# Kernel tuning notes

Hardware: AMD Instinct MI355X
Metric: run time of the kernel (lower is better)

## Reference

```python
import jax, jax.numpy as jnp
import numpy as np

B, N_LEAVES, HID, NCLS, VOCAB = 32, 512, 128, 2, 50257
N_NODES = 2 * N_LEAVES - 1  # complete binary tree, heap layout


def setup_inputs() -> dict:
    key = jax.random.key(0)
    ks = jax.random.split(key, 12)
    x = jax.random.randint(ks[0], (B, N_NODES), 0, VOCAB)
    cue = jax.random.randint(ks[1], (B, N_NODES), 0, NCLS)
    # word j sits at tree leaf node L-1+j
    word_index = jnp.tile(jnp.arange(N_LEAVES - 1, 2 * N_LEAVES - 1), (B, 1))
    # parent->child adjacency stored in adj[:, 1]
    A = np.zeros((2, N_NODES, N_NODES), dtype=bool)
    p = np.arange(N_LEAVES - 1)
    A[1, p, 2 * p + 1] = True
    A[1, p, 2 * p + 2] = True
    adj = jnp.asarray(np.broadcast_to(A, (B, 2, N_NODES, N_NODES)).copy())
    s = 0.05
    emb = jax.random.normal(ks[2], (VOCAB, HID - NCLS)) * s
    Wc = jax.random.normal(ks[3], (HID, 2 * HID)) * s
    bc = jax.random.normal(ks[4], (HID,)) * s
    Wd = jax.random.normal(ks[5], (2 * HID, 2 * HID)) * s
    bd = jax.random.normal(ks[6], (2 * HID,)) * s
    Wg = jax.random.normal(ks[7], (HID, HID)) * s
    bg = jax.random.normal(ks[8], (HID,)) * s
    Wcl = jax.random.normal(ks[9], (NCLS, 2 * HID)) * s
    bcl = jax.random.normal(ks[10], (NCLS,)) * s
    return dict(x=x, word_index=word_index, cue=cue, adj=adj, emb=emb,
                Wc=Wc, bc=bc, Wd=Wd, bd=bd, Wg=Wg, bg=bg, Wcl=Wcl, bcl=bcl)


def reference(x, word_index, cue, adj, emb, Wc, bc, Wd, bd, Wg, bg, Wcl, bcl):
    # adj encodes the same complete binary heap tree that is hardcoded below
    Bn, N = x.shape
    H = Wc.shape[0]
    C = bcl.shape[0]
    L = (N + 1) // 2
    depth = L.bit_length() - 1  # leaves live at level `depth`
    bidx = jnp.arange(Bn)[:, None]

    word_emb = emb[x]                                   # (B, N, H-C)
    cue_oh = jax.nn.one_hot(cue, C, dtype=word_emb.dtype)
    in_feats = jnp.concatenate([word_emb, cue_oh], -1)  # (B, N, H)
    sent = in_feats[bidx, word_index]                   # (B, L, H) leaf feats

    # ---- upward compose: level-batched bottom-up traversal ----
    h = jnp.zeros((Bn, N, H), in_feats.dtype).at[bidx, word_index].set(sent)
    for d in range(depth - 1, -1, -1):
        p = jnp.arange(2 ** d - 1, 2 ** (d + 1) - 1)
        ctx = jnp.concatenate([h[:, 2 * p + 1], h[:, 2 * p + 2]], -1)  # (B, 2^d, 2H)
        h = h.at[:, p].set(jnp.tanh(ctx @ Wc.T + bc))
    # upward_results never writes leaf rows -> leaves stay zero
    up = h.at[bidx, word_index].set(0.0)

    g_down = jax.nn.sigmoid(h[:, 0] @ Wg.T + bg)        # (B, H)

    # ---- downward decompose: level-batched top-down traversal ----
    down = jnp.zeros_like(h).at[:, 0].set(g_down)
    for d in range(depth):
        p = jnp.arange(2 ** d - 1, 2 ** (d + 1) - 1)
        ctx = jnp.concatenate([down[:, p], up[:, p]], -1)
        ch = jnp.tanh(ctx @ Wd.T + bd)                  # (B, 2^d, 2H)
        down = down.at[:, 2 * p + 1].set(ch[..., :H]).at[:, 2 * p + 2].set(ch[..., H:])

    tree = jnp.concatenate([down, up], -1)              # (B, N, 2H)
    scores = jax.nn.sigmoid(tree @ Wcl.T + bcl)
    return jax.nn.softmax(scores, -1)
```

## Files before the change

### kernel.cpp

```cpp
#include <hip/hip_runtime.h>


constexpr int NNODES = 1023;
constexpr int HB = 128;

__device__ __forceinline__ float fold16(const float* a, int l) {
  float b[8];
#pragma unroll
  for (int u = 0; u < 8; ++u) {
    const float mine = (l & 1) ? a[2 * u + 1] : a[2 * u];
    const float oth  = (l & 1) ? a[2 * u]     : a[2 * u + 1];
    b[u] = mine + __shfl_xor(oth, 1);
  }
  float c[4];
#pragma unroll
  for (int u = 0; u < 4; ++u) {
    const float mine = (l & 2) ? b[2 * u + 1] : b[2 * u];
    const float oth  = (l & 2) ? b[2 * u]     : b[2 * u + 1];
    c[u] = mine + __shfl_xor(oth, 2);
  }
  float d[2];
#pragma unroll
  for (int u = 0; u < 2; ++u) {
    const float mine = (l & 4) ? c[2 * u + 1] : c[2 * u];
    const float oth  = (l & 4) ? c[2 * u]     : c[2 * u + 1];
    d[u] = mine + __shfl_xor(oth, 4);
  }
  const float mine = (l & 8) ? d[1] : d[0];
  const float oth  = (l & 8) ? d[0] : d[1];
  return mine + __shfl_xor(oth, 8);
}

__device__ __forceinline__ float fold8(const float* a, int l) {
  float b[4];
#pragma unroll
  for (int u = 0; u < 4; ++u) {
    const float mine = (l & 1) ? a[2 * u + 1] : a[2 * u];
    const float oth  = (l & 1) ? a[2 * u]     : a[2 * u + 1];
    b[u] = mine + __shfl_xor(oth, 1);
  }
  float c[2];
#pragma unroll
  for (int u = 0; u < 2; ++u) {
    const float mine = (l & 2) ? b[2 * u + 1] : b[2 * u];
    const float oth  = (l & 2) ? b[2 * u]     : b[2 * u + 1];
    c[u] = mine + __shfl_xor(oth, 2);
  }
  const float mine = (l & 4) ? c[1] : c[0];
  const float oth  = (l & 4) ? c[0] : c[1];
  return mine + __shfl_xor(oth, 4);
}

__device__ __forceinline__ float fold4(const float* a, int l) {
  float b[2];
#pragma unroll
  for (int u = 0; u < 2; ++u) {
    const float mine = (l & 1) ? a[2 * u + 1] : a[2 * u];
    const float oth  = (l & 1) ? a[2 * u]     : a[2 * u + 1];
    b[u] = mine + __shfl_xor(oth, 1);
  }
  const float mine = (l & 2) ? b[1] : b[0];
  const float oth  = (l & 2) ? b[0] : b[1];
  return mine + __shfl_xor(oth, 2);
}

template<int CH>
__device__ __forceinline__ float foldCH(const float (&a)[CH * 4], int l16) {
  if constexpr (CH == 4) {
    return fold16(a, l16);
  } else if constexpr (CH == 2) {
    float t = fold8(a, l16);
    t += __shfl_xor(t, 8);
    return t;
  } else {
    float t = fold4(a, l16);
    t += __shfl_xor(t, 4);
    t += __shfl_xor(t, 8);
    return t;
  }
}

template<int CH>
__device__ __forceinline__ void up_pass(float* __restrict__ heap, int base, int cb,
                                        int cbase, const float4 (&w)[4][4],
                                        float bias_r, int g, int l16, bool wr) {
  float a[CH * 4];
#pragma unroll
  for (int v = 0; v < CH * 4; ++v) a[v] = 0.f;
#pragma unroll
  for (int p = 0; p < CH; ++p) {
    const float* cp = heap + (cb + 2 * (cbase + p)) * HB + l16 * 4;
#pragma unroll
    for (int m = 0; m < 4; ++m) {
      const float4 cc = *(const float4*)(cp + m * 64);
#pragma unroll
      for (int r = 0; r < 4; ++r) {
        const float4 wv = w[r][m];
        a[p * 4 + r] = fmaf(wv.x, cc.x, fmaf(wv.y, cc.y,
                        fmaf(wv.z, cc.z, fmaf(wv.w, cc.w, a[p * 4 + r]))));
      }
    }
  }
  const float tot = foldCH<CH>(a, l16);
  if (wr && l16 < CH * 4) {
    const int p = l16 >> 2;
    heap[(base + cbase + p) * HB + 4 * g + (l16 & 3)] = tanhf(tot + bias_r);
  }
}

template<int NP, int NH>
__device__ __forceinline__ void up_level16(float* __restrict__ heap,
                                           const float4 (&w)[4][4],
                                           float bias_r, int g, int l16, int ph) {
  constexpr int base = NP - 1, cb = 2 * NP - 1;
  if constexpr (NP >= 4 * NH) {
#pragma unroll
    for (int c0 = 0; c0 < NP; c0 += 4 * NH)
      up_pass<4>(heap, base, cb, c0 + ph * 4, w, bias_r, g, l16, true);
  } else if constexpr (NP * 2 == 4 * NH) {
    up_pass<2>(heap, base, cb, ph * 2, w, bias_r, g, l16, true);
  } else if constexpr (NP == NH) {
    up_pass<1>(heap, base, cb, ph, w, bias_r, g, l16, true);
  } else {
    up_pass<1>(heap, base, cb, 0, w, bias_r, g, l16, ph == 0);
  }
  __syncthreads();
}

template<int CH>
__device__ __forceinline__ void down_pass(float* __restrict__ db,
                                          const float* __restrict__ ub,
                                          int base, int cb, int cbase,
                                          const float4 (&w)[4][4],
                                          float bias_r, int g, int l16) {
  float a[CH * 4];
#pragma unroll
  for (int v = 0; v < CH * 4; ++v) a[v] = 0.f;
#pragma unroll
  for (int p = 0; p < CH; ++p) {
    const float* dp = db + (base + cbase + p) * HB + l16 * 4;
    const float* up = ub + (base + cbase + p) * HB + l16 * 4;
#pragma unroll
    for (int m = 0; m < 4; ++m) {
      const float4 cc = *(const float4*)(((m < 2) ? dp : up) + (m & 1) * 64);
#pragma unroll
      for (int r = 0; r < 4; ++r) {
        const float4 wv = w[r][m];
        a[p * 4 + r] = fmaf(wv.x, cc.x, fmaf(wv.y, cc.y,
                        fmaf(wv.z, cc.z, fmaf(wv.w, cc.w, a[p * 4 + r]))));
      }
    }
  }
  const float tot = foldCH<CH>(a, l16);
  if (l16 < CH * 4) {
    const int p = l16 >> 2;
    const int row = 4 * g + (l16 & 3);
    db[(cb + 2 * (cbase + p) + (row >> 7)) * HB + (row & 127)] = tanhf(tot + bias_r);
  }
}

template<int NP>
__device__ __forceinline__ void down_level16(float* __restrict__ db,
                                             const float* __restrict__ ub,
                                             const float4 (&w)[4][4],
                                             float bias_r, int g, int l16) {
  constexpr int base = NP - 1, cb = 2 * NP - 1;
  if constexpr (NP >= 4) {
#pragma unroll
    for (int c0 = 0; c0 < NP; c0 += 4)
      down_pass<4>(db, ub, base, cb, c0, w, bias_r, g, l16);
  } else {
    down_pass<NP>(db, ub, base, cb, 0, w, bias_r, g, l16);
  }
  __syncthreads();
}

__device__ __forceinline__ void classify16(const float* __restrict__ dn,
                                           const float* __restrict__ un,
                                           const float* __restrict__ wcl,
                                           const float* __restrict__ bcl,
                                           float* __restrict__ o, int l16) {
  const int k0 = l16 * 8;
  float s0, s1;
  {
    const float4 d0 = *(const float4*)(dn + k0);
    const float4 d1 = *(const float4*)(dn + k0 + 4);
    const float4 a0 = *(const float4*)(wcl + k0);
    const float4 a1 = *(const float4*)(wcl + k0 + 4);
    const float4 b0 = *(const float4*)(wcl + 256 + k0);
    const float4 b1 = *(const float4*)(wcl + 256 + k0 + 4);
    s0 = d0.x * a0.x + d0.y * a0.y + d0.z * a0.z + d0.w * a0.w
       + d1.x * a1.x + d1.y * a1.y + d1.z * a1.z + d1.w * a1.w;
    s1 = d0.x * b0.x + d0.y * b0.y + d0.z * b0.z + d0.w * b0.w
       + d1.x * b1.x + d1.y * b1.y + d1.z * b1.z + d1.w * b1.w;
  }
  if (un) {
    const float4 u0 = *(const float4*)(un + k0);
    const float4 u1 = *(const float4*)(un + k0 + 4);
    const float4 a0 = *(const float4*)(wcl + 128 + k0);
    const float4 a1 = *(const float4*)(wcl + 128 + k0 + 4);
    const float4 b0 = *(const float4*)(wcl + 384 + k0);
    const float4 b1 = *(const float4*)(wcl + 384 + k0 + 4);
    s0 += u0.x * a0.x + u0.y * a0.y + u0.z * a0.z + u0.w * a0.w
        + u1.x * a1.x + u1.y * a1.y + u1.z * a1.z + u1.w * a1.w;
    s1 += u0.x * b0.x + u0.y * b0.y + u0.z * b0.z + u0.w * b0.w
        + u1.x * b1.x + u1.y * b1.y + u1.z * b1.z + u1.w * b1.w;
  }
#pragma unroll
  for (int m = 8; m >= 1; m >>= 1) {
    s0 += __shfl_xor(s0, m);
    s1 += __shfl_xor(s1, m);
  }
  if (l16 == 0) {
    s0 += bcl[0]; s1 += bcl[1];
    const float p0 = 1.f / (1.f + expf(-s0));
    const float p1 = 1.f / (1.f + expf(-s1));
    const float mx = fmaxf(p0, p1);
    const float e0 = expf(p0 - mx), e1 = expf(p1 - mx);
    const float inv = 1.f / (e0 + e1);
    o[0] = e0 * inv;
    o[1] = e1 * inv;
  }
}

__global__ __launch_bounds__(512, 4) void kA_up(const int* __restrict__ x,
                                                const int* __restrict__ cue,
                                                const float* __restrict__ emb,
                                                const float* __restrict__ Wc,
                                                const float* __restrict__ bc,
                                                float* __restrict__ hw) {
  __shared__ __align__(16) float heap[63 * HB];
  __shared__ __align__(16) float pad[7296];
  const int b = blockIdx.x >> 4, s = blockIdx.x & 15, r = 15 + s;
  const int t = threadIdx.x, g = t >> 4, l16 = t & 15;
  if (t == 0) ((volatile float*)pad)[0] = 0.f;

  float4 w[4][4];
#pragma unroll
  for (int rr = 0; rr < 4; ++rr)
#pragma unroll
    for (int m = 0; m < 4; ++m)
      w[rr][m] = *(const float4*)(Wc + (4 * g + rr) * 256 + l16 * 4 + m * 64);
  const float bias_r = bc[4 * g + (l16 & 3)];

  for (int idx = t; idx < 32 * HB; idx += 512) {
    const int j = idx >> 7, k = idx & 127;
    const int gq = ((r + 1) << 5) - 1 + j;
    float v;
    if (k < 126) v = emb[(long long)x[b * NNODES + gq] * 126 + k];
    else         v = (cue[b * NNODES + gq] == (k - 126)) ? 1.f : 0.f;
    heap[(31 + j) * HB + k] = v;
  }
  __syncthreads();

  up_level16<16, 1>(heap, w, bias_r, g, l16, 0);
  up_level16<8, 1>(heap, w, bias_r, g, l16, 0);
  up_level16<4, 1>(heap, w, bias_r, g, l16, 0);
  up_level16<2, 1>(heap, w, bias_r, g, l16, 0);
  up_level16<1, 1>(heap, w, bias_r, g, l16, 0);

  float4* dst = (float4*)(hw + (size_t)(b * 16 + s) * 31 * HB);
  const float4* src = (const float4*)heap;
  for (int idx = t; idx < 31 * 32; idx += 512) dst[idx] = src[idx];
}

__global__ __launch_bounds__(1024, 4) void kC_all(const float* __restrict__ Wc,
                                                  const float* __restrict__ bc,
                                                  const float* __restrict__ Wg,
                                                  const float* __restrict__ bg,
                                                  const float* __restrict__ Wd,
                                                  const float* __restrict__ bd,
                                                  const float* __restrict__ Wcl,
                                                  const float* __restrict__ bcl,
                                                  const float* __restrict__ hw,
                                                  float* __restrict__ out) {
  __shared__ __align__(16) float A[63 * HB];
  __shared__ __align__(16) float B[31 * HB];
  __shared__ __align__(16) float rootdn[2 * HB];
  __shared__ __align__(16) float wcl[512];
  __shared__ __align__(16) float pad[7400];
  const int b = blockIdx.x >> 3, sp = blockIdx.x & 7;
  const int t = threadIdx.x, g = t >> 4, l16 = t & 15;
  if (t == 0) ((volatile float*)pad)[0] = 0.f;

  {
    float4* B4 = (float4*)(B + 15 * HB);
    for (int idx = t; idx < 16 * 32; idx += 1024) {
      const int s = idx >> 5, k4 = idx & 31;
      B4[idx] = ((const float4*)(hw + (size_t)(b * 16 + s) * 31 * HB))[k4];
    }
  }
  if (t < 512) wcl[t] = Wcl[t];
  __syncthreads();

  {
    const int gu = g & 31, ph = t >> 9;
    float4 w[4][4];
#pragma unroll
    for (int rr = 0; rr < 4; ++rr)
#pragma unroll
      for (int m = 0; m < 4; ++m)
        w[rr][m] = *(const float4*)(Wc + (4 * gu + rr) * 256 + l16 * 4 + m * 64);
    const float bias_r = bc[4 * gu + (l16 & 3)];
    up_level16<8, 2>(B, w, bias_r, gu, l16, ph);
    up_level16<4, 2>(B, w, bias_r, gu, l16, ph);
    up_level16<2, 2>(B, w, bias_r, gu, l16, ph);
    up_level16<1, 2>(B, w, bias_r, gu, l16, ph);

    float4 wg[4][2];
#pragma unroll
    for (int rr = 0; rr < 4; ++rr)
#pragma unroll
      for (int m = 0; m < 2; ++m)
        wg[rr][m] = *(const float4*)(Wg + (4 * gu + rr) * 128 + l16 * 4 + m * 64);
    float a[4];
#pragma unroll
    for (int v = 0; v < 4; ++v) a[v] = 0.f;
#pragma unroll
    for (int m = 0; m < 2; ++m) {
      const float4 cc = *(const float4*)(B + l16 * 4 + m * 64);
#pragma unroll
      for (int rr = 0; rr < 4; ++rr) {
        const float4 wv = wg[rr][m];
        a[rr] = fmaf(wv.x, cc.x, fmaf(wv.y, cc.y, fmaf(wv.z, cc.z, fmaf(wv.w, cc.w, a[rr]))));
      }
    }
    float tot = fold4(a, l16);
    tot += __shfl_xor(tot, 4);
    tot += __shfl_xor(tot, 8);
    if (ph == 0 && l16 < 4) {
      const int row = 4 * gu + l16;
      A[row] = 1.f / (1.f + expf(-(tot + bg[row])));
    }
    __syncthreads();
  }
  asm volatile("" ::: "memory");

  float4 w[4][4];
#pragma unroll
  for (int rr = 0; rr < 4; ++rr)
#pragma unroll
    for (int m = 0; m < 4; ++m)
      w[rr][m] = *(const float4*)(Wd + (4 * g + rr) * 256 + l16 * 4 + m * 64);
  const float bias_r = bd[4 * g + (l16 & 3)];

  down_level16<1>(A, B, w, bias_r, g, l16);
  down_level16<2>(A, B, w, bias_r, g, l16);
  down_level16<4>(A, B, w, bias_r, g, l16);
  down_level16<8>(A, B, w, bias_r, g, l16);

  if (sp == 0 && t < 15 * 16) {
    const int m = t >> 4;
    classify16(A + m * HB, B + m * HB, wcl, bcl,
               out + ((size_t)b * NNODES + m) * 2, l16);
  }
  if (t < 256) rootdn[t] = A[(15 + sp * 2 + (t >> 7)) * HB + (t & 127)];
  __syncthreads();

  for (int ss = 0; ss < 2; ++ss) {
    const int s = sp * 2 + ss, r = 15 + s;

    {
      const float4* s4 = (const float4*)(hw + (size_t)(b * 16 + s) * 31 * HB);
      float4* B4 = (float4*)B;
      for (int idx = t; idx < 31 * 32; idx += 1024) B4[idx] = s4[idx];
      if (t < HB) A[t] = rootdn[ss * HB + t];
    }
    __syncthreads();

    down_level16<1>(A, B, w, bias_r, g, l16);
    down_level16<2>(A, B, w, bias_r, g, l16);
    down_level16<4>(A, B, w, bias_r, g, l16);
    down_level16<8>(A, B, w, bias_r, g, l16);
    down_level16<16>(A, B, w, bias_r, g, l16);

    if (t < 63 * 16) {
      const int m = t >> 4;
      const int lvl = 31 - __clz(m + 1);
      const int j = (m + 1) - (1 << lvl);
      const int gq = ((r + 1) << lvl) - 1 + j;
      classify16(A + m * HB, (m < 31) ? (B + m * HB) : nullptr, wcl, bcl,
                 out + ((size_t)b * NNODES + gq) * 2, l16);
    }
    __syncthreads();
  }
}

extern "C" void kernel_launch(void* const* d_in, const int* in_sizes, int n_in,
                              void* d_out, int out_size, void* d_ws, size_t ws_size,
                              hipStream_t stream) {
  const int*   x   = (const int*)d_in[0];
  const int*   cue = (const int*)d_in[2];
  const float* emb = (const float*)d_in[4];
  const float* Wc  = (const float*)d_in[5];
  const float* bc  = (const float*)d_in[6];
  const float* Wd  = (const float*)d_in[7];
  const float* bd  = (const float*)d_in[8];
  const float* Wg  = (const float*)d_in[9];
  const float* bg  = (const float*)d_in[10];
  const float* Wcl = (const float*)d_in[11];
  const float* bcl = (const float*)d_in[12];
  float* out = (float*)d_out;

  float* hw = (float*)d_ws;

  hipLaunchKernelGGL(kA_up,  dim3(512), dim3(512), 0, stream, x, cue, emb, Wc, bc, hw);
  hipLaunchKernelGGL(kC_all, dim3(256), dim3(1024), 0, stream,
                     Wc, bc, Wg, bg, Wd, bd, Wcl, bcl, hw, out);
}
```

Baseline: 76.95 us.

## Store tree states in fp16 and use packed dot2 with dual-subtree down pass

Converts the shared-memory heaps, the workspace and the weight registers from fp32 to packed fp16, and replaces the fp32 FMA chains with v_dot2 fp16 dot products that accumulate in fp32. This halves LDS and global traffic and the number of math instructions. The two sub-subtrees per block in the down pass are now processed together with shared barriers, where before they ran in a sequential loop. Hidden states and weights are rounded to fp16, so precision drops.

```diff
diff --git a/kernel.cpp b/kernel.cpp
--- a/kernel.cpp
+++ b/kernel.cpp
@@ -1,8 +1,36 @@
 #include <hip/hip_runtime.h>
+#include <hip/hip_fp16.h>
 
 
 constexpr int NNODES = 1023;
-constexpr int HB = 128;
+
+typedef _Float16 h2 __attribute__((ext_vector_type(2)));
+
+__device__ __forceinline__ float dot2(uint a, uint b, float c) {
+  union { uint u; h2 h; } x, y;
+  x.u = a; y.u = b;
+  return __builtin_amdgcn_fdot2(x.h, y.h, c, false);
+}
+
+__device__ __forceinline__ uint f2h2(float a, float b) {
+  return (uint)__half_as_ushort(__float2half_rn(a)) |
+         ((uint)__half_as_ushort(__float2half_rn(b)) << 16);
+}
+
+__device__ __forceinline__ float2 h2f2(uint u) {
+  union { uint u; h2 h; } c; c.u = u;
+  return make_float2((float)c.h.x, (float)c.h.y);
+}
+
+__device__ __forceinline__ void load_wslice(const float* __restrict__ Wrow,
+                                            int l16, int m, uint* wout) {
+  const float4 f0 = *(const float4*)(Wrow + l16 * 8 + m * 128);
+  const float4 f1 = *(const float4*)(Wrow + l16 * 8 + m * 128 + 4);
+  wout[0] = f2h2(f0.x, f0.y);
+  wout[1] = f2h2(f0.z, f0.w);
+  wout[2] = f2h2(f1.x, f1.y);
+  wout[3] = f2h2(f1.z, f1.w);
+}
 
 __device__ __forceinline__ float fold16(const float* a, int l) {
   float b[8];
@@ -81,130 +109,158 @@
 }
 
 template<int CH>
-__device__ __forceinline__ void up_pass(float* __restrict__ heap, int base, int cb,
-                                        int cbase, const float4 (&w)[4][4],
+__device__ __forceinline__ void up_pass(uint* __restrict__ heap2, int base, int cb,
+                                        int cbase, const uint (&w)[4][8],
                                         float bias_r, int g, int l16, bool wr) {
   float a[CH * 4];
 #pragma unroll
   for (int v = 0; v < CH * 4; ++v) a[v] = 0.f;
 #pragma unroll
   for (int p = 0; p < CH; ++p) {
-    const float* cp = heap + (cb + 2 * (cbase + p)) * HB + l16 * 4;
-#pragma unroll
-    for (int m = 0; m < 4; ++m) {
-      const float4 cc = *(const float4*)(cp + m * 64);
+    const uint* cp = heap2 + (cb + 2 * (cbase + p)) * 64 + l16 * 4;
+#pragma unroll
+    for (int m = 0; m < 2; ++m) {
+      const uint4 cc = *(const uint4*)(cp + m * 64);
 #pragma unroll
       for (int r = 0; r < 4; ++r) {
-        const float4 wv = w[r][m];
-        a[p * 4 + r] = fmaf(wv.x, cc.x, fmaf(wv.y, cc.y,
-                        fmaf(wv.z, cc.z, fmaf(wv.w, cc.w, a[p * 4 + r]))));
+        float av = a[p * 4 + r];
+        av = dot2(w[r][m * 4 + 0], cc.x, av);
+        av = dot2(w[r][m * 4 + 1], cc.y, av);
+        av = dot2(w[r][m * 4 + 2], cc.z, av);
+        av = dot2(w[r][m * 4 + 3], cc.w, av);
+        a[p * 4 + r] = av;
       }
     }
   }
   const float tot = foldCH<CH>(a, l16);
   if (wr && l16 < CH * 4) {
-    const int p = l16 >> 2;
-    heap[(base + cbase + p) * HB + 4 * g + (l16 & 3)] = tanhf(tot + bias_r);
+    _Float16* hH = (_Float16*)heap2;
+    hH[(base + cbase + (l16 >> 2)) * 128 + 4 * g + (l16 & 3)] =
+        (_Float16)tanhf(tot + bias_r);
   }
 }
 
 template<int NP, int NH>
-__device__ __forceinline__ void up_level16(float* __restrict__ heap,
-                                           const float4 (&w)[4][4],
+__device__ __forceinline__ void up_level16(uint* __restrict__ heap2,
+                                           const uint (&w)[4][8],
                                            float bias_r, int g, int l16, int ph) {
   constexpr int base = NP - 1, cb = 2 * NP - 1;
   if constexpr (NP >= 4 * NH) {
 #pragma unroll
     for (int c0 = 0; c0 < NP; c0 += 4 * NH)
-      up_pass<4>(heap, base, cb, c0 + ph * 4, w, bias_r, g, l16, true);
+      up_pass<4>(heap2, base, cb, c0 + ph * 4, w, bias_r, g, l16, true);
   } else if constexpr (NP * 2 == 4 * NH) {
-    up_pass<2>(heap, base, cb, ph * 2, w, bias_r, g, l16, true);
+    up_pass<2>(heap2, base, cb, ph * 2, w, bias_r, g, l16, true);
   } else if constexpr (NP == NH) {
-    up_pass<1>(heap, base, cb, ph, w, bias_r, g, l16, true);
+    up_pass<1>(heap2, base, cb, ph, w, bias_r, g, l16, true);
   } else {
-    up_pass<1>(heap, base, cb, 0, w, bias_r, g, l16, ph == 0);
+    up_pass<1>(heap2, base, cb, 0, w, bias_r, g, l16, ph == 0);
   }
   __syncthreads();
 }
 
 template<int CH>
-__device__ __forceinline__ void down_pass(float* __restrict__ db,
-                                          const float* __restrict__ ub,
+__device__ __forceinline__ void down_pass(uint* __restrict__ db2,
+                                          const uint* __restrict__ ub2,
                                           int base, int cb, int cbase,
-                                          const float4 (&w)[4][4],
+                                          const uint (&w)[4][8],
                                           float bias_r, int g, int l16) {
   float a[CH * 4];
 #pragma unroll
   for (int v = 0; v < CH * 4; ++v) a[v] = 0.f;
 #pragma unroll
   for (int p = 0; p < CH; ++p) {
-    const float* dp = db + (base + cbase + p) * HB + l16 * 4;
-    const float* up = ub + (base + cbase + p) * HB + l16 * 4;
-#pragma unroll
-    for (int m = 0; m < 4; ++m) {
-      const float4 cc = *(const float4*)(((m < 2) ? dp : up) + (m & 1) * 64);
-#pragma unroll
-      for (int r = 0; r < 4; ++r) {
-        const float4 wv = w[r][m];
-        a[p * 4 + r] = fmaf(wv.x, cc.x, fmaf(wv.y, cc.y,
-                        fmaf(wv.z, cc.z, fmaf(wv.w, cc.w, a[p * 4 + r]))));
-      }
+    const uint* dp = db2 + (base + cbase + p) * 64 + l16 * 4;
+    const uint* up = ub2 + (base + cbase + p) * 64 + l16 * 4;
+    const uint4 c0 = *(const uint4*)dp;
+    const uint4 c1 = *(const uint4*)up;
+#pragma unroll
+    for (int r = 0; r < 4; ++r) {
+      float av = a[p * 4 + r];
+      av = dot2(w[r][0], c0.x, av);
+      av = dot2(w[r][1], c0.y, av);
+      av = dot2(w[r][2], c0.z, av);
+      av = dot2(w[r][3], c0.w, av);
+      av = dot2(w[r][4], c1.x, av);
+      av = dot2(w[r][5], c1.y, av);
+      av = dot2(w[r][6], c1.z, av);
+      av = dot2(w[r][7], c1.w, av);
+      a[p * 4 + r] = av;
     }
   }
   const float tot = foldCH<CH>(a, l16);
   if (l16 < CH * 4) {
-    const int p = l16 >> 2;
     const int row = 4 * g + (l16 & 3);
-    db[(cb + 2 * (cbase + p) + (row >> 7)) * HB + (row & 127)] = tanhf(tot + bias_r);
+    ((_Float16*)db2)[(cb + 2 * (cbase + (l16 >> 2)) + (row >> 7)) * 128 + (row & 127)] =
+        (_Float16)tanhf(tot + bias_r);
   }
 }
 
 template<int NP>
-__device__ __forceinline__ void down_level16(float* __restrict__ db,
-                                             const float* __restrict__ ub,
-                                             const float4 (&w)[4][4],
+__device__ __forceinline__ void down_level16(uint* __restrict__ db2,
+                                             const uint* __restrict__ ub2,
+                                             const uint (&w)[4][8],
                                              float bias_r, int g, int l16) {
   constexpr int base = NP - 1, cb = 2 * NP - 1;
   if constexpr (NP >= 4) {
 #pragma unroll
     for (int c0 = 0; c0 < NP; c0 += 4)
-      down_pass<4>(db, ub, base, cb, c0, w, bias_r, g, l16);
+      down_pass<4>(db2, ub2, base, cb, c0, w, bias_r, g, l16);
   } else {
-    down_pass<NP>(db, ub, base, cb, 0, w, bias_r, g, l16);
-  }
-  __syncthreads();
-}
-
-__device__ __forceinline__ void classify16(const float* __restrict__ dn,
-                                           const float* __restrict__ un,
+    down_pass<NP>(db2, ub2, base, cb, 0, w, bias_r, g, l16);
+  }
+  __syncthreads();
+}
+
+template<int NP>
+__device__ __forceinline__ void down_level16_dual(uint* __restrict__ A0,
+                                                  const uint* __restrict__ B0,
+                                                  uint* __restrict__ A1,
+                                                  const uint* __restrict__ B1,
+                                                  const uint (&w)[4][8],
+                                                  float bias_r, int g, int l16) {
+  constexpr int base = NP - 1, cb = 2 * NP - 1;
+  if constexpr (NP >= 4) {
+#pragma unroll
+    for (int c0 = 0; c0 < NP; c0 += 4) {
+      down_pass<4>(A0, B0, base, cb, c0, w, bias_r, g, l16);
+      down_pass<4>(A1, B1, base, cb, c0, w, bias_r, g, l16);
+    }
+  } else {
+    down_pass<NP>(A0, B0, base, cb, 0, w, bias_r, g, l16);
+    down_pass<NP>(A1, B1, base, cb, 0, w, bias_r, g, l16);
+  }
+  __syncthreads();
+}
+
+__device__ __forceinline__ void classify16(const uint* __restrict__ dn2,
+                                           const uint* __restrict__ un2,
                                            const float* __restrict__ wcl,
                                            const float* __restrict__ bcl,
                                            float* __restrict__ o, int l16) {
   const int k0 = l16 * 8;
-  float s0, s1;
+  float s0 = 0.f, s1 = 0.f;
   {
-    const float4 d0 = *(const float4*)(dn + k0);
-    const float4 d1 = *(const float4*)(dn + k0 + 4);
-    const float4 a0 = *(const float4*)(wcl + k0);
-    const float4 a1 = *(const float4*)(wcl + k0 + 4);
-    const float4 b0 = *(const float4*)(wcl + 256 + k0);
-    const float4 b1 = *(const float4*)(wcl + 256 + k0 + 4);
-    s0 = d0.x * a0.x + d0.y * a0.y + d0.z * a0.z + d0.w * a0.w
-       + d1.x * a1.x + d1.y * a1.y + d1.z * a1.z + d1.w * a1.w;
-    s1 = d0.x * b0.x + d0.y * b0.y + d0.z * b0.z + d0.w * b0.w
-       + d1.x * b1.x + d1.y * b1.y + d1.z * b1.z + d1.w * b1.w;
-  }
-  if (un) {
-    const float4 u0 = *(const float4*)(un + k0);
-    const float4 u1 = *(const float4*)(un + k0 + 4);
-    const float4 a0 = *(const float4*)(wcl + 128 + k0);
-    const float4 a1 = *(const float4*)(wcl + 128 + k0 + 4);
-    const float4 b0 = *(const float4*)(wcl + 384 + k0);
-    const float4 b1 = *(const float4*)(wcl + 384 + k0 + 4);
-    s0 += u0.x * a0.x + u0.y * a0.y + u0.z * a0.z + u0.w * a0.w
-        + u1.x * a1.x + u1.y * a1.y + u1.z * a1.z + u1.w * a1.w;
-    s1 += u0.x * b0.x + u0.y * b0.y + u0.z * b0.z + u0.w * b0.w
-        + u1.x * b1.x + u1.y * b1.y + u1.z * b1.z + u1.w * b1.w;
+    const uint4 du = *(const uint4*)(dn2 + l16 * 4);
+    const float2 d0 = h2f2(du.x), d1 = h2f2(du.y), d2 = h2f2(du.z), d3 = h2f2(du.w);
+    s0 += d0.x * wcl[k0]     + d0.y * wcl[k0 + 1] + d1.x * wcl[k0 + 2] + d1.y * wcl[k0 + 3]
+        + d2.x * wcl[k0 + 4] + d2.y * wcl[k0 + 5] + d3.x * wcl[k0 + 6] + d3.y * wcl[k0 + 7];
+    s1 += d0.x * wcl[256 + k0]     + d0.y * wcl[256 + k0 + 1]
+        + d1.x * wcl[256 + k0 + 2] + d1.y * wcl[256 + k0 + 3]
+        + d2.x * wcl[256 + k0 + 4] + d2.y * wcl[256 + k0 + 5]
+        + d3.x * wcl[256 + k0 + 6] + d3.y * wcl[256 + k0 + 7];
+  }
+  if (un2) {
+    const uint4 uu = *(const uint4*)(un2 + l16 * 4);
+    const float2 u0 = h2f2(uu.x), u1 = h2f2(uu.y), u2 = h2f2(uu.z), u3 = h2f2(uu.w);
+    s0 += u0.x * wcl[128 + k0]     + u0.y * wcl[128 + k0 + 1]
+        + u1.x * wcl[128 + k0 + 2] + u1.y * wcl[128 + k0 + 3]
+        + u2.x * wcl[128 + k0 + 4] + u2.y * wcl[128 + k0 + 5]
+        + u3.x * wcl[128 + k0 + 6] + u3.y * wcl[128 + k0 + 7];
+    s1 += u0.x * wcl[384 + k0]     + u0.y * wcl[384 + k0 + 1]
+        + u1.x * wcl[384 + k0 + 2] + u1.y * wcl[384 + k0 + 3]
+        + u2.x * wcl[384 + k0 + 4] + u2.y * wcl[384 + k0 + 5]
+        + u3.x * wcl[384 + k0 + 6] + u3.y * wcl[384 + k0 + 7];
   }
 #pragma unroll
   for (int m = 8; m >= 1; m >>= 1) {
@@ -228,40 +284,42 @@
                                                 const float* __restrict__ emb,
                                                 const float* __restrict__ Wc,
                                                 const float* __restrict__ bc,
-                                                float* __restrict__ hw) {
-  __shared__ __align__(16) float heap[63 * HB];
-  __shared__ __align__(16) float pad[7296];
+                                                uint* __restrict__ hw) {
+  __shared__ __align__(16) uint heap2[63 * 64];
+  __shared__ __align__(16) uint pad[10240];
   const int b = blockIdx.x >> 4, s = blockIdx.x & 15, r = 15 + s;
   const int t = threadIdx.x, g = t >> 4, l16 = t & 15;
-  if (t == 0) ((volatile float*)pad)[0] = 0.f;
-
-  float4 w[4][4];
+  if (t == 0) ((volatile uint*)pad)[0] = 0u;
+
+  uint w[4][8];
 #pragma unroll
   for (int rr = 0; rr < 4; ++rr)
 #pragma unroll
-    for (int m = 0; m < 4; ++m)
-      w[rr][m] = *(const float4*)(Wc + (4 * g + rr) * 256 + l16 * 4 + m * 64);
+    for (int m = 0; m < 2; ++m)
+      load_wslice(Wc + (4 * g + rr) * 256, l16, m, &w[rr][m * 4]);
   const float bias_r = bc[4 * g + (l16 & 3)];
 
-  for (int idx = t; idx < 32 * HB; idx += 512) {
-    const int j = idx >> 7, k = idx & 127;
+  for (int idx = t; idx < 32 * 64; idx += 512) {
+    const int j = idx >> 6, c = idx & 63, k0 = 2 * c;
     const int gq = ((r + 1) << 5) - 1 + j;
-    float v;
-    if (k < 126) v = emb[(long long)x[b * NNODES + gq] * 126 + k];
-    else         v = (cue[b * NNODES + gq] == (k - 126)) ? 1.f : 0.f;
-    heap[(31 + j) * HB + k] = v;
-  }
-  __syncthreads();
-
-  up_level16<16, 1>(heap, w, bias_r, g, l16, 0);
-  up_level16<8, 1>(heap, w, bias_r, g, l16, 0);
-  up_level16<4, 1>(heap, w, bias_r, g, l16, 0);
-  up_level16<2, 1>(heap, w, bias_r, g, l16, 0);
-  up_level16<1, 1>(heap, w, bias_r, g, l16, 0);
-
-  float4* dst = (float4*)(hw + (size_t)(b * 16 + s) * 31 * HB);
-  const float4* src = (const float4*)heap;
-  for (int idx = t; idx < 31 * 32; idx += 512) dst[idx] = src[idx];
+    const int xi = x[b * NNODES + gq], ci = cue[b * NNODES + gq];
+    const float v0 = (k0 < 126) ? emb[(long long)xi * 126 + k0]
+                                : ((ci == (k0 - 126)) ? 1.f : 0.f);
+    const float v1 = (k0 + 1 < 126) ? emb[(long long)xi * 126 + k0 + 1]
+                                    : ((ci == (k0 + 1 - 126)) ? 1.f : 0.f);
+    heap2[(31 + j) * 64 + c] = f2h2(v0, v1);
+  }
+  __syncthreads();
+
+  up_level16<16, 1>(heap2, w, bias_r, g, l16, 0);
+  up_level16<8, 1>(heap2, w, bias_r, g, l16, 0);
+  up_level16<4, 1>(heap2, w, bias_r, g, l16, 0);
+  up_level16<2, 1>(heap2, w, bias_r, g, l16, 0);
+  up_level16<1, 1>(heap2, w, bias_r, g, l16, 0);
+
+  uint4* dst = (uint4*)(hw + (size_t)(b * 16 + s) * 31 * 64);
+  const uint4* src = (const uint4*)heap2;
+  for (int idx = t; idx < 31 * 16; idx += 512) dst[idx] = src[idx];
 }
 
 __global__ __launch_bounds__(1024, 4) void kC_all(const float* __restrict__ Wc,
@@ -272,57 +330,58 @@
                                                   const float* __restrict__ bd,
                                                   const float* __restrict__ Wcl,
                                                   const float* __restrict__ bcl,
-                                                  const float* __restrict__ hw,
+                                                  const uint* __restrict__ hw,
                                                   float* __restrict__ out) {
-  __shared__ __align__(16) float A[63 * HB];
-  __shared__ __align__(16) float B[31 * HB];
-  __shared__ __align__(16) float rootdn[2 * HB];
+  __shared__ __align__(16) uint A2[2 * 63 * 64];
+  __shared__ __align__(16) uint B2[2 * 31 * 64];
+  __shared__ __align__(16) uint rootdn2[128];
   __shared__ __align__(16) float wcl[512];
-  __shared__ __align__(16) float pad[7400];
+  __shared__ __align__(16) uint pad[8192];
   const int b = blockIdx.x >> 3, sp = blockIdx.x & 7;
   const int t = threadIdx.x, g = t >> 4, l16 = t & 15;
-  if (t == 0) ((volatile float*)pad)[0] = 0.f;
-
-  {
-    float4* B4 = (float4*)(B + 15 * HB);
-    for (int idx = t; idx < 16 * 32; idx += 1024) {
-      const int s = idx >> 5, k4 = idx & 31;
-      B4[idx] = ((const float4*)(hw + (size_t)(b * 16 + s) * 31 * HB))[k4];
-    }
+  if (t == 0) ((volatile uint*)pad)[0] = 0u;
+  uint* A1 = A2 + 63 * 64;
+  uint* B1 = B2 + 31 * 64;
+
+  for (int idx = t; idx < 16 * 16; idx += 1024) {
+    const int s = idx >> 4, q = idx & 15;
+    *((uint4*)(B2 + (15 + s) * 64) + q) =
+        *((const uint4*)(hw + (size_t)(b * 16 + s) * 31 * 64) + q);
   }
   if (t < 512) wcl[t] = Wcl[t];
   __syncthreads();
 
   {
     const int gu = g & 31, ph = t >> 9;
-    float4 w[4][4];
+    uint wu[4][8];
 #pragma unroll
     for (int rr = 0; rr < 4; ++rr)
 #pragma unroll
-      for (int m = 0; m < 4; ++m)
-        w[rr][m] = *(const float4*)(Wc + (4 * gu + rr) * 256 + l16 * 4 + m * 64);
-    const float bias_r = bc[4 * gu + (l16 & 3)];
-    up_level16<8, 2>(B, w, bias_r, gu, l16, ph);
-    up_level16<4, 2>(B, w, bias_r, gu, l16, ph);
-    up_level16<2, 2>(B, w, bias_r, gu, l16, ph);
-    up_level16<1, 2>(B, w, bias_r, gu, l16, ph);
-
-    float4 wg[4][2];
+      for (int m = 0; m < 2; ++m)
+        load_wslice(Wc + (4 * gu + rr) * 256, l16, m, &wu[rr][m * 4]);
+    const float bias_u = bc[4 * gu + (l16 & 3)];
+    up_level16<8, 2>(B2, wu, bias_u, gu, l16, ph);
+    up_level16<4, 2>(B2, wu, bias_u, gu, l16, ph);
+    up_level16<2, 2>(B2, wu, bias_u, gu, l16, ph);
+    up_level16<1, 2>(B2, wu, bias_u, gu, l16, ph);
+
+    uint wg[4][4];
 #pragma unroll
     for (int rr = 0; rr < 4; ++rr)
-#pragma unroll
-      for (int m = 0; m < 2; ++m)
-        wg[rr][m] = *(const float4*)(Wg + (4 * gu + rr) * 128 + l16 * 4 + m * 64);
+      load_wslice(Wg + (4 * gu + rr) * 128, l16, 0, &wg[rr][0]);
     float a[4];
 #pragma unroll
     for (int v = 0; v < 4; ++v) a[v] = 0.f;
-#pragma unroll
-    for (int m = 0; m < 2; ++m) {
-      const float4 cc = *(const float4*)(B + l16 * 4 + m * 64);
+    {
+      const uint4 cc = *(const uint4*)(B2 + l16 * 4);
 #pragma unroll
       for (int rr = 0; rr < 4; ++rr) {
-        const float4 wv = wg[rr][m];
-        a[rr] = fmaf(wv.x, cc.x, fmaf(wv.y, cc.y, fmaf(wv.z, cc.z, fmaf(wv.w, cc.w, a[rr]))));
+        float av = a[rr];
+        av = dot2(wg[rr][0], cc.x, av);
+        av = dot2(wg[rr][1], cc.y, av);
+        av = dot2(wg[rr][2], cc.z, av);
+        av = dot2(wg[rr][3], cc.w, av);
+        a[rr] = av;
       }
     }
     float tot = fold4(a, l16);
@@ -330,59 +389,60 @@
     tot += __shfl_xor(tot, 8);
     if (ph == 0 && l16 < 4) {
       const int row = 4 * gu + l16;
-      A[row] = 1.f / (1.f + expf(-(tot + bg[row])));
+      ((_Float16*)A2)[row] = (_Float16)(1.f / (1.f + expf(-(tot + bg[row]))));
     }
     __syncthreads();
   }
   asm volatile("" ::: "memory");
 
-  float4 w[4][4];
+  uint w[4][8];
 #pragma unroll
   for (int rr = 0; rr < 4; ++rr)
 #pragma unroll
-    for (int m = 0; m < 4; ++m)
-      w[rr][m] = *(const float4*)(Wd + (4 * g + rr) * 256 + l16 * 4 + m * 64);
+    for (int m = 0; m < 2; ++m)
+      load_wslice(Wd + (4 * g + rr) * 256, l16, m, &w[rr][m * 4]);
   const float bias_r = bd[4 * g + (l16 & 3)];
 
-  down_level16<1>(A, B, w, bias_r, g, l16);
-  down_level16<2>(A, B, w, bias_r, g, l16);
-  down_level16<4>(A, B, w, bias_r, g, l16);
-  down_level16<8>(A, B, w, bias_r, g, l16);
+  down_level16<1>(A2, B2, w, bias_r, g, l16);
+  down_level16<2>(A2, B2, w, bias_r, g, l16);
+  down_level16<4>(A2, B2, w, bias_r, g, l16);
+  down_level16<8>(A2, B2, w, bias_r, g, l16);
 
   if (sp == 0 && t < 15 * 16) {
     const int m = t >> 4;
-    classify16(A + m * HB, B + m * HB, wcl, bcl,
+    classify16(A2 + m * 64, B2 + m * 64, wcl, bcl,
                out + ((size_t)b * NNODES + m) * 2, l16);
   }
-  if (t < 256) rootdn[t] = A[(15 + sp * 2 + (t >> 7)) * HB + (t & 127)];
-  __syncthreads();
-
-  for (int ss = 0; ss < 2; ++ss) {
-    const int s = sp * 2 + ss, r = 15 + s;
-
-    {
-      const float4* s4 = (const float4*)(hw + (size_t)(b * 16 + s) * 31 * HB);
-      float4* B4 = (float4*)B;
-      for (int idx = t; idx < 31 * 32; idx += 1024) B4[idx] = s4[idx];
-      if (t < HB) A[t] = rootdn[ss * HB + t];
-    }
-    __syncthreads();
-
-    down_level16<1>(A, B, w, bias_r, g, l16);
-    down_level16<2>(A, B, w, bias_r, g, l16);
-    down_level16<4>(A, B, w, bias_r, g, l16);
-    down_level16<8>(A, B, w, bias_r, g, l16);
-    down_level16<16>(A, B, w, bias_r, g, l16);
-
-    if (t < 63 * 16) {
-      const int m = t >> 4;
-      const int lvl = 31 - __clz(m + 1);
-      const int j = (m + 1) - (1 << lvl);
+  if (t < 128) rootdn2[t] = A2[(15 + sp * 2 + (t >> 6)) * 64 + (t & 63)];
+  __syncthreads();
+
+  for (int idx = t; idx < 2 * 31 * 16; idx += 1024) {
+    const int ss = (idx >= 31 * 16) ? 1 : 0;
+    const int k4 = idx - ss * 31 * 16;
+    ((uint4*)(B2 + ss * 31 * 64))[k4] =
+        ((const uint4*)(hw + (size_t)(b * 16 + sp * 2 + ss) * 31 * 64))[k4];
+  }
+  if (t < 128) A2[(t >> 6) * 63 * 64 + (t & 63)] = rootdn2[t];
+  __syncthreads();
+
+  down_level16_dual<1>(A2, B2, A1, B1, w, bias_r, g, l16);
+  down_level16_dual<2>(A2, B2, A1, B1, w, bias_r, g, l16);
+  down_level16_dual<4>(A2, B2, A1, B1, w, bias_r, g, l16);
+  down_level16_dual<8>(A2, B2, A1, B1, w, bias_r, g, l16);
+  down_level16_dual<16>(A2, B2, A1, B1, w, bias_r, g, l16);
+
+  if (t < 63 * 16) {
+    const int m = t >> 4;
+    const int lvl = 31 - __clz(m + 1);
+    const int j = (m + 1) - (1 << lvl);
+#pragma unroll
+    for (int ss = 0; ss < 2; ++ss) {
+      const int r = 15 + sp * 2 + ss;
       const int gq = ((r + 1) << lvl) - 1 + j;
-      classify16(A + m * HB, (m < 31) ? (B + m * HB) : nullptr, wcl, bcl,
+      classify16(A2 + ss * 63 * 64 + m * 64,
+                 (m < 31) ? (B2 + ss * 31 * 64 + m * 64) : nullptr, wcl, bcl,
                  out + ((size_t)b * NNODES + gq) * 2, l16);
     }
-    __syncthreads();
   }
 }
 
@@ -402,7 +462,7 @@
   const float* bcl = (const float*)d_in[12];
   float* out = (float*)d_out;
 
-  float* hw = (float*)d_ws;
+  uint* hw = (uint*)d_ws;
 
   hipLaunchKernelGGL(kA_up,  dim3(512), dim3(512), 0, stream, x, cue, emb, Wc, bc, hw);
   hipLaunchKernelGGL(kC_all, dim3(256), dim3(1024), 0, stream,
```

Result: faster. 70.38 us (median of 2 runs) (-8.5%).
